# Kernel tuning notes

Measured on AMD Instinct MI355X. Metric: run time of the kernel, lower is better.

Reference implementation:

```python
import jax, jax.numpy as jnp
import numpy as np
from jax import lax

SCALES = [0.5, 0.25, 0.125, 0.0625]
D_MODEL = 256
IN_CH = 1


def setup_inputs() -> dict:
    key = jax.random.key(0)
    ks = jax.random.split(key, 16)
    x = jax.random.normal(ks[0], (2, D_MODEL, 256, 256), dtype=jnp.float32)
    m = jax.random.uniform(ks[1], (2, IN_CH, 256, 256), dtype=jnp.float32)
    s = 0.05
    Wq = jax.random.normal(ks[2], (D_MODEL, D_MODEL, 1, 1), jnp.float32) * s
    bq = jax.random.normal(ks[3], (D_MODEL,), jnp.float32) * s
    Wk = jax.random.normal(ks[4], (D_MODEL, D_MODEL, 1, 1), jnp.float32) * s
    bk = jax.random.normal(ks[5], (D_MODEL,), jnp.float32) * s
    Wv = jax.random.normal(ks[6], (D_MODEL, D_MODEL, 1, 1), jnp.float32) * s
    bv = jax.random.normal(ks[7], (D_MODEL,), jnp.float32) * s
    Wmq = jax.random.normal(ks[8], (D_MODEL, IN_CH, 1, 1), jnp.float32) * s
    bmq = jax.random.normal(ks[9], (D_MODEL,), jnp.float32) * s
    Wmk = jax.random.normal(ks[10], (D_MODEL, IN_CH, 1, 1), jnp.float32) * s
    bmk = jax.random.normal(ks[11], (D_MODEL,), jnp.float32) * s
    Wo = jax.random.normal(ks[12], (D_MODEL, D_MODEL, 3, 3), jnp.float32) * s
    bo = jax.random.normal(ks[13], (D_MODEL,), jnp.float32) * s
    return {"x": x, "m": m, "Wq": Wq, "bq": bq, "Wk": Wk, "bk": bk,
            "Wv": Wv, "bv": bv, "Wmq": Wmq, "bmq": bmq, "Wmk": Wmk, "bmk": bmk,
            "Wo": Wo, "bo": bo, "b": 1, "c": 256}


def _conv1x1(z, W, bias):
    # W: (O, I, 1, 1)
    return jnp.einsum('bihw,oi->bohw', z, W[:, :, 0, 0]) + bias[None, :, None, None]


def _forward(x, m, Wq, bq, Wk, bk, Wv, bv, Wmq, bmq, Wmk, bmk, Wo, bo, b, c):
    bt, _, h, w = x.shape  # h, w are multiples of 64 -> pad is zero
    t = bt // b
    n_scales = len(SCALES)
    d_k = c // n_scales

    q = _conv1x1(x, Wq, bq)
    k = _conv1x1(x, Wk, bk)
    v = _conv1x1(x, Wv, bv)
    mq = _conv1x1(m, Wmq, bmq)
    mk = _conv1x1(m, Wmk, bmk)

    outs = []
    for i, scale in enumerate(SCALES):
        height, width = int(h * scale), int(w * scale)
        out_h, out_w = h // height, w // width
        sl = slice(i * d_k, (i + 1) * d_k)

        def patch(z):
            # (b, t, d_k, out_h, height, out_w, width) -> (b, t*out_h*out_w, d_k*height*width)
            z = z[:, sl].reshape(b, t, d_k, out_h, height, out_w, width)
            z = z.transpose(0, 1, 3, 5, 2, 4, 6)
            return z.reshape(b, t * out_h * out_w, d_k * height * width)

        Q, K, V = patch(q), patch(k), patch(v)
        MQ, MK = patch(mq), patch(mk)
        inv_sqrt_d = 1.0 / jnp.sqrt(jnp.asarray(Q.shape[-1], jnp.float32))
        scores = jnp.einsum('bnd,bmd->bnm', Q, K) * inv_sqrt_d
        mask_scores = jnp.einsum('bnd,bmd->bnm', MQ, MK) * inv_sqrt_d
        p_attn = jax.nn.softmax(scores * mask_scores, axis=-1)
        y = jnp.einsum('bnm,bmd->bnd', p_attn, V)
        # back to (bt, d_k, h, w)
        y = y.reshape(b, t, out_h, out_w, d_k, height, width)
        y = y.transpose(0, 1, 4, 2, 5, 3, 6).reshape(bt, d_k, h, w)
        outs.append(y)

    out = jnp.concatenate(outs, axis=1)
    z = lax.conv_general_dilated(out, Wo, window_strides=(1, 1),
                                 padding=((1, 1), (1, 1)),
                                 dimension_numbers=('NCHW', 'OIHW', 'NCHW'))
    z = z + bo[None, :, None, None]
    return jnp.where(z > 0, z, 0.2 * z)  # LeakyReLU(0.2)


def reference(x, m, Wq, bq, Wk, bk, Wv, bv, Wmq, bmq, Wmk, bmk, Wo, bo, b, c):
    return _forward(x, m, Wq, bq, Wk, bk, Wv, bv, Wmq, bmq, Wmk, bmk, Wo, bo, b, c)
```

## Files before the change

### kernel.cpp

```cpp
#include <hip/hip_runtime.h>
#include <stdint.h>


typedef __attribute__((ext_vector_type(8))) short short8;
typedef __attribute__((ext_vector_type(4))) float floatx4;
typedef __attribute__((ext_vector_type(4))) unsigned int uintx4;

#define DEV static __device__ __forceinline__

DEV unsigned short f2bf(float f) {
  unsigned u = __builtin_bit_cast(unsigned, f);
  unsigned r = u + 0x7FFFu + ((u >> 16) & 1u);
  return (unsigned short)(r >> 16);
}

DEV void patch_row(int n, int sc, int lw, int& pt, int& sp0) {
  pt = n >> (2 + 2 * sc);
  int rem = n & ((4 << (2 * sc)) - 1);
  int oh = rem >> (1 + sc), ow = rem & ((2 << sc) - 1);
  sp0 = (oh << (lw + 8)) + (ow << lw);
}

__global__ void k_prep_w(const float* __restrict__ Wq, const float* __restrict__ Wk,
                         const float* __restrict__ Wv, const float* __restrict__ bq,
                         const float* __restrict__ bk, const float* __restrict__ bv,
                         const float* __restrict__ Wmq, const float* __restrict__ bmq,
                         const float* __restrict__ Wmk, const float* __restrict__ bmk,
                         unsigned short* __restrict__ wqkv, float* __restrict__ bias,
                         float* __restrict__ msc) {
  int b = blockIdx.x;
  int t = threadIdx.x;
  if (b < 768) {
    const float* src = b < 256 ? (Wq + b * 256) : (b < 512 ? (Wk + (b - 256) * 256)
                                                           : (Wv + (b - 512) * 256));
    wqkv[b * 256 + t] = f2bf(src[t]);
    if (t == 0) bias[b] = b < 256 ? bq[b] : (b < 512 ? bk[b - 256] : bv[b - 512]);
  } else {
    int sc = t >> 6, lane = t & 63;
    int ch = sc * 64 + lane;
    float a0 = Wmq[ch] * Wmk[ch];
    float a1 = Wmq[ch] * bmk[ch];
    float a2 = bmq[ch] * Wmk[ch];
    float a3 = bmq[ch] * bmk[ch];
    for (int off = 32; off; off >>= 1) {
      a0 += __shfl_xor(a0, off); a1 += __shfl_xor(a1, off);
      a2 += __shfl_xor(a2, off); a3 += __shfl_xor(a3, off);
    }
    if (lane == 0) {
      msc[sc * 4 + 0] = a0; msc[sc * 4 + 1] = a1;
      msc[sc * 4 + 2] = a2; msc[sc * 4 + 3] = a3;
    }
  }
}

__global__ void k_prep_wo(const float* __restrict__ Wo, unsigned short* __restrict__ wobf,
                          float* __restrict__ scoresG, unsigned int* __restrict__ pbuf) {
  int blk = blockIdx.x;
  if (blk < 2304) {
    int didx = blk >> 8, o = blk & 255, c = threadIdx.x;
    wobf[didx * 65536 + o * 256 + c] = f2bf(Wo[o * 2304 + c * 9 + didx]);
  } else {
    int i = (blk - 2304) * 256 + threadIdx.x;
    if (i < 559232) scoresG[i] = 0.f;
    if (i < 140032) pbuf[i] = 0u;
  }
}

__global__ __launch_bounds__(256) void k_xt(const float* __restrict__ x,
                                            unsigned short* __restrict__ xt) {
  __shared__ __align__(16) unsigned short tile[64][72];
  int p0 = blockIdx.x * 64, c0 = blockIdx.y * 64, t = blockIdx.z;
  int tid = threadIdx.x;
  {
    int cc = tid >> 2, pq = (tid & 3) * 16;
    const float* src = x + ((t * 256 + c0 + cc) * 65536 + p0 + pq);
    __align__(16) unsigned short tmp[16];
#pragma unroll
    for (int e = 0; e < 16; e += 4) {
      floatx4 v = *(const floatx4*)(src + e);
      tmp[e + 0] = f2bf(v[0]); tmp[e + 1] = f2bf(v[1]);
      tmp[e + 2] = f2bf(v[2]); tmp[e + 3] = f2bf(v[3]);
    }
    *(uintx4*)&tile[cc][pq] = *(const uintx4*)&tmp[0];
    *(uintx4*)&tile[cc][pq + 8] = *(const uintx4*)&tmp[8];
  }
  __syncthreads();
  {
    int pp = tid >> 2, cg = (tid & 3) * 16;
    __align__(16) unsigned short outv[16];
#pragma unroll
    for (int e = 0; e < 16; ++e) outv[e] = tile[cg + e][pp];
    unsigned short* dst = xt + ((t * 65536 + p0 + pp) * 256 + c0 + cg);
    *(uintx4*)dst = *(const uintx4*)&outv[0];
    *(uintx4*)(dst + 8) = *(const uintx4*)&outv[8];
  }
}

__global__ __launch_bounds__(256) void k_yt(const unsigned short* __restrict__ ynat,
                                            unsigned short* __restrict__ yt) {
  __shared__ __align__(16) unsigned short tile[64][72];
  int p0 = blockIdx.x * 64, c0 = blockIdx.y * 64, t = blockIdx.z;
  int tid = threadIdx.x;
  {
    int cc = tid >> 2, pq = (tid & 3) * 16;
    const unsigned short* src = ynat + ((t * 256 + c0 + cc) * 65536 + p0 + pq);
    *(uintx4*)&tile[cc][pq] = *(const uintx4*)src;
    *(uintx4*)&tile[cc][pq + 8] = *(const uintx4*)(src + 8);
  }
  __syncthreads();
  {
    int pp = tid >> 2, cg = (tid & 3) * 16;
    __align__(16) unsigned short outv[16];
#pragma unroll
    for (int e = 0; e < 16; ++e) outv[e] = tile[cg + e][pp];
    unsigned short* dst = yt + ((t * 65536 + p0 + pp) * 256 + c0 + cg);
    *(uintx4*)dst = *(const uintx4*)&outv[0];
    *(uintx4*)(dst + 8) = *(const uintx4*)&outv[8];
  }
}

__global__ __launch_bounds__(256) void k_qkv(const unsigned short* __restrict__ xt,
                                             const unsigned short* __restrict__ wqkv,
                                             const float* __restrict__ bias,
                                             unsigned short* __restrict__ qkv) {
  __shared__ __align__(16) unsigned short As[128][64];
  __shared__ __align__(16) unsigned short Bs[128][64];
  int flat = blockIdx.x + (blockIdx.y << 10);
  int lg = ((flat & 7) * 768) + (flat >> 3);
  int n_t = lg / 6, m_t = lg - n_t * 6;
  int n0 = n_t << 7, m0 = m_t << 7;
  int tid = threadIdx.x;
  int w = tid >> 6, l = tid & 63;
  int wr = w >> 1, wc = w & 1;
  int l15 = l & 15, lhi = l >> 4;
  int sr = tid >> 1, sbase = (tid & 1) * 4, r7 = sr & 7;
  const unsigned short* gA = wqkv + (m0 + sr) * 256 + sbase * 8;
  const unsigned short* gB = xt + (n0 + sr) * 256 + sbase * 8;
  floatx4 zf = {0.f, 0.f, 0.f, 0.f};
  floatx4 acc[4][4];
#pragma unroll
  for (int i = 0; i < 4; ++i)
#pragma unroll
    for (int j = 0; j < 4; ++j) acc[i][j] = zf;
  uintx4 ra[4], rb[4];
#define QLOAD(K0) { const uintx4* pa = (const uintx4*)(gA + (K0)); \
                    const uintx4* pb = (const uintx4*)(gB + (K0)); \
                    ra[0] = pa[0]; ra[1] = pa[1]; ra[2] = pa[2]; ra[3] = pa[3]; \
                    rb[0] = pb[0]; rb[1] = pb[1]; rb[2] = pb[2]; rb[3] = pb[3]; }
  QLOAD(0);
#pragma unroll
  for (int ch = 0; ch < 4; ++ch) {
    __syncthreads();
#pragma unroll
    for (int j = 0; j < 4; ++j) {
      *(uintx4*)&As[sr][((sbase + j) ^ r7) * 8] = ra[j];
      *(uintx4*)&Bs[sr][((sbase + j) ^ r7) * 8] = rb[j];
    }
    __syncthreads();
    if (ch < 3) QLOAD((ch + 1) * 64);
#pragma unroll
    for (int kk = 0; kk < 2; ++kk) {
      short8 af[4], bfr[4];
#pragma unroll
      for (int f = 0; f < 4; ++f) {
        int arow = wr * 64 + f * 16 + l15;
        af[f] = *(const short8*)&As[arow][(((kk << 2) + lhi) ^ (arow & 7)) * 8];
        int brow = wc * 64 + f * 16 + l15;
        bfr[f] = *(const short8*)&Bs[brow][(((kk << 2) + lhi) ^ (brow & 7)) * 8];
      }
#pragma unroll
      for (int fm = 0; fm < 4; ++fm)
#pragma unroll
        for (int fn = 0; fn < 4; ++fn)
          acc[fm][fn] = __builtin_amdgcn_mfma_f32_16x16x32_bf16(af[fm], bfr[fn], acc[fm][fn], 0, 0, 0);
    }
  }
#undef QLOAD
#pragma unroll
  for (int fm = 0; fm < 4; ++fm) {
    int crow = m0 + wr * 64 + fm * 16 + lhi * 4;
#pragma unroll
    for (int rr = 0; rr < 4; ++rr) {
      float bv = bias[crow + rr];
#pragma unroll
      for (int fn = 0; fn < 4; ++fn) {
        int pcol = n0 + wc * 64 + fn * 16 + l15;
        int t = pcol >> 16, p = pcol & 65535;
        qkv[(t * 768 + crow + rr) * 65536 + p] = f2bf(acc[fm][fn][rr] + bv);
      }
    }
  }
}

__global__ __launch_bounds__(256) void k_gram2(const float* __restrict__ m,
                                               float* __restrict__ G) {
  __shared__ __align__(16) float Ns[32][68];
  __shared__ __align__(16) float Ms[32][68];
  int bid = blockIdx.x;
  int sc, tn, tm, z, nchunks, soff;
  if (bid < 32)      { sc = 0; tn = 0; tm = 0; z = bid;      nchunks = 8; soff = 0; }
  else if (bid < 40) { sc = 1; tn = 0; tm = 0; z = bid - 32; nchunks = 8; soff = 64; }
  else if (bid < 72) { int r = bid - 40; int tl = r >> 1; sc = 2; tn = tl >> 2; tm = tl & 3; z = r & 1; nchunks = 8; soff = 1088; }
  else               { int tl = bid - 72; sc = 3; tn = tl >> 4; tm = tl & 15; z = 0; nchunks = 4; soff = 17472; }
  int lw = 7 - sc, W = 1 << lw, N = 8 << (2 * sc);
  int kbase = z * nchunks * 64;
  int n0 = tn * 32, m0 = tm * 32;
  int tid = threadIdx.x;
  bool isA = tid < 128;
  int u = tid & 127;
  int srow = u >> 2, sslot0 = (u & 3) * 4;
  int grow = (isA ? n0 : m0) + srow;
  bool valid = grow < N;
  int pt = 0, sp0 = 0;
  if (valid) patch_row(grow, sc, lw, pt, sp0);
  int gbase = pt * 65536 + sp0;
  int trc = tid >> 4, tcc = tid & 15;
  float a00 = 0.f, a01 = 0.f, a10 = 0.f, a11 = 0.f;
  floatx4 zf = {0.f, 0.f, 0.f, 0.f};
  for (int c = 0; c < nchunks; ++c) {
    int k0 = kbase + c * 64;
    floatx4 v[4];
#pragma unroll
    for (int j = 0; j < 4; ++j) {
      v[j] = zf;
      if (valid) {
        int s = k0 + (sslot0 + j) * 4;
        int hh = s >> lw, ww = s & (W - 1);
        v[j] = *(const floatx4*)(m + gbase + (hh << 8) + ww);
      }
    }
    __syncthreads();
    float* dstrow = isA ? &Ns[srow][0] : &Ms[srow][0];
#pragma unroll
    for (int j = 0; j < 4; ++j) *(floatx4*)&dstrow[(sslot0 + j) * 4] = v[j];
    __syncthreads();
#pragma unroll 4
    for (int k = 0; k < 64; k += 4) {
      floatx4 na = *(const floatx4*)&Ns[2 * trc][k];
      floatx4 nb = *(const floatx4*)&Ns[2 * trc + 1][k];
      floatx4 ma = *(const floatx4*)&Ms[2 * tcc][k];
      floatx4 mb = *(const floatx4*)&Ms[2 * tcc + 1][k];
#pragma unroll
      for (int e = 0; e < 4; ++e) {
        a00 += na[e] * ma[e]; a01 += na[e] * mb[e];
        a10 += nb[e] * ma[e]; a11 += nb[e] * mb[e];
      }
    }
  }
  int rn = n0 + 2 * trc, rm = m0 + 2 * tcc;
  float res[2][2] = {{a00, a01}, {a10, a11}};
#pragma unroll
  for (int i = 0; i < 2; ++i)
#pragma unroll
    for (int j = 0; j < 2; ++j) {
      if (rn + i < N && rm + j < N) {
        float* dst = &G[soff + (rn + i) * N + rm + j];
        if (sc < 3) atomicAdd(dst, res[i][j]); else *dst = res[i][j];
      }
    }
}

__global__ void k_rsum(const float* __restrict__ m, float* __restrict__ rbuf) {
  int row = blockIdx.x, lane = threadIdx.x;
  int sc, n;
  if (row < 8)        { sc = 0; n = row; }
  else if (row < 40)  { sc = 1; n = row - 8; }
  else if (row < 168) { sc = 2; n = row - 40; }
  else                { sc = 3; n = row - 168; }
  int lw = 7 - sc, W = 1 << lw;
  int pt, sp0;
  patch_row(n, sc, lw, pt, sp0);
  int base = pt * 65536 + sp0;
  int S = 1 << (14 - 2 * sc);
  float acc = 0.f;
  for (int s = lane; s < S; s += 64) {
    int hh = s >> lw, ww = s & (W - 1);
    acc += m[base + (hh << 8) + ww];
  }
  for (int off = 32; off; off >>= 1) acc += __shfl_xor(acc, off);
  if (lane == 0) rbuf[row] = acc;
}

__global__ __launch_bounds__(256) void k_scores2(const unsigned short* __restrict__ qkv,
                                                 float* __restrict__ scores) {
  __shared__ __align__(16) unsigned short As[32][136];
  __shared__ __align__(16) unsigned short Bs[32][136];
  int bid = blockIdx.x;
  int sc, tn, tm, z, soff;
  if (bid < 256)      { sc = 0; tn = 0; tm = 0; z = bid;       soff = 0; }
  else if (bid < 320) { sc = 1; tn = 0; tm = 0; z = bid - 256; soff = 64; }
  else if (bid < 576) { int r = bid - 320; int tl = r >> 4; sc = 2; tn = tl >> 2; tm = tl & 3; z = r & 15; soff = 1088; }
  else                { int r = bid - 576; int tl = r >> 2; sc = 3; tn = tl >> 4; tm = tl & 15; z = r & 3; soff = 17472; }
  int lw = 7 - sc, W = 1 << lw, lS = 14 - 2 * sc, N = 8 << (2 * sc);
  int n0 = tn * 32, m0 = tm * 32;
  int kbase = z * 4096;
  int tid = threadIdx.x, w = tid >> 6, l = tid & 63;
  int wr = w >> 1, wc = w & 1, l15 = l & 15, lhi = l >> 4;
  floatx4 acc = {0.f, 0.f, 0.f, 0.f};
  bool isA = tid < 128;
  int u = tid & 127;
  int srow = u >> 2, sslot0 = (u & 3) * 4;
  int grow = (isA ? n0 : m0) + srow;
  int cb = (isA ? 0 : 256) + sc * 64;
  int pt = 0, sp0 = 0;
  bool valid = grow < N;
  if (valid) patch_row(grow, sc, lw, pt, sp0);
  int rowbase = (pt * 768 + cb) * 65536 + sp0;
  uintx4 zu = {0u, 0u, 0u, 0u};
  uintx4 r[4];
#define SLOAD(KS) { int kb2 = kbase + (KS) * 128; \
  _Pragma("unroll") for (int j = 0; j < 4; ++j) { \
    uintx4 v = zu; \
    if (valid) { int k = kb2 + (sslot0 + j) * 8; \
      int cl = k >> lS; int s = k & ((1 << lS) - 1); \
      int hh = s >> lw, ww = s & (W - 1); \
      v = *(const uintx4*)(qkv + rowbase + cl * 65536 + (hh << 8) + ww); } \
    r[j] = v; } }
  SLOAD(0);
  for (int ks = 0; ks < 32; ++ks) {
    __syncthreads();
    {
      unsigned short* dstrow = isA ? &As[srow][0] : &Bs[srow][0];
#pragma unroll
      for (int j = 0; j < 4; ++j) *(uintx4*)&dstrow[(sslot0 + j) * 8] = r[j];
    }
    __syncthreads();
    if (ks < 31) SLOAD(ks + 1);
#pragma unroll
    for (int kk = 0; kk < 4; ++kk) {
      short8 a = *(const short8*)&As[wr * 16 + l15][(kk * 4 + lhi) * 8];
      short8 b = *(const short8*)&Bs[wc * 16 + l15][(kk * 4 + lhi) * 8];
      acc = __builtin_amdgcn_mfma_f32_16x16x32_bf16(a, b, acc, 0, 0, 0);
    }
  }
#undef SLOAD
  int rrow = n0 + wr * 16 + lhi * 4;
  int ccol = m0 + wc * 16 + l15;
  if (ccol < N) {
#pragma unroll
    for (int rr = 0; rr < 4; ++rr)
      if (rrow + rr < N) atomicAdd(&scores[soff + (rrow + rr) * N + ccol], acc[rr]);
  }
}

__global__ void k_softmax(const float* __restrict__ scores, const float* __restrict__ G,
                          const float* __restrict__ rbuf, const float* __restrict__ msc,
                          unsigned short* __restrict__ pbuf) {
  int row = blockIdx.x, lane = threadIdx.x;
  int sc, n, roff, soff, poff;
  if (row < 8)        { sc = 0; n = row;       roff = 0;   soff = 0;     poff = 0; }
  else if (row < 40)  { sc = 1; n = row - 8;   roff = 8;   soff = 64;    poff = 512; }
  else if (row < 168) { sc = 2; n = row - 40;  roff = 40;  soff = 1088;  poff = 1536; }
  else                { sc = 3; n = row - 168; roff = 168; soff = 17472; poff = 17920; }
  int N = 8 << (2 * sc);
  int Kpad = (sc < 2) ? 32 : N;
  float Sf = (float)(1 << (14 - 2 * sc));
  float invD = 1.0f / (float)(1 << (20 - 2 * sc));
  float alpha = msc[sc * 4 + 0], beta = msc[sc * 4 + 1];
  float gamma = msc[sc * 4 + 2], delta = msc[sc * 4 + 3];
  float rn = rbuf[roff + n];
  float vals[8];
  float mx = -1e30f;
#pragma unroll
  for (int j = 0; j < 8; ++j) {
    float v = -1e30f;
    int mcol = lane + j * 64;
    if (j * 64 < N && mcol < N) {
      float sq = scores[soff + n * N + mcol];
      float g = G[soff + n * N + mcol];
      float rm = rbuf[roff + mcol];
      v = sq * (alpha * g + beta * rn + gamma * rm + delta * Sf) * invD;
    }
    vals[j] = v;
    mx = fmaxf(mx, v);
  }
  for (int off = 32; off; off >>= 1) mx = fmaxf(mx, __shfl_xor(mx, off));
  float sum = 0.f;
#pragma unroll
  for (int j = 0; j < 8; ++j) {
    int mcol = lane + j * 64;
    float e = 0.f;
    if (j * 64 < N && mcol < N) e = __expf(vals[j] - mx);
    vals[j] = e;
    sum += e;
  }
  for (int off = 32; off; off >>= 1) sum += __shfl_xor(sum, off);
  float inv = 1.f / sum;
#pragma unroll
  for (int j = 0; j < 8; ++j) {
    int mcol = lane + j * 64;
    if (j * 64 < N && mcol < N) pbuf[poff + n * Kpad + mcol] = f2bf(vals[j] * inv);
  }
}

__global__ __launch_bounds__(256) void k_pv(const unsigned short* __restrict__ qkv,
                                            const unsigned short* __restrict__ pbuf,
                                            unsigned short* __restrict__ ynat) {
  int bid = blockIdx.x;
  int sc, bx, by;
  if (bid < 4096)      { sc = 0; bx = bid; by = 0; }
  else if (bid < 6144) { sc = 1; bx = bid - 4096; by = 0; }
  else if (bid < 8192) { int r = bid - 6144; sc = 2; bx = r >> 1; by = r & 1; }
  else                 { int r = bid - 8192; sc = 3; bx = r >> 3; by = r & 7; }
  int WR    = (sc == 0) ? 1 : (sc == 1) ? 2 : 4;
  int logWC = (sc == 0) ? 2 : (sc == 1) ? 1 : 0;
  int poff  = (sc == 0) ? 0 : (sc == 1) ? 512 : (sc == 2) ? 1536 : 17920;
  int lw = 7 - sc, W = 1 << lw;
  int lS = 14 - 2 * sc;
  int N = 8 << (2 * sc);
  int Kpad = (sc < 2) ? 32 : N;
  int WC = 1 << logWC;
  int d0 = bx * (WC * 64);
  int nb = by * (WR * 16);
  __shared__ __align__(16) unsigned short As[64][40];
  __shared__ __align__(16) unsigned short Bt[256][32];
  int tid = threadIdx.x;
  int w = tid >> 6, l = tid & 63;
  int wr = w >> logWC, wc = w & (WC - 1);
  int l15 = l & 15, lhi = l >> 4;
  floatx4 zf = {0.f, 0.f, 0.f, 0.f};
  floatx4 acc[4];
#pragma unroll
  for (int i = 0; i < 4; ++i) acc[i] = zf;
  int bmp = tid & 15;
  int dg = tid >> 4;
  bool act0 = (WC > 1) || (dg < 8);
  bool has1 = (WC == 4);
  bool doA = tid < WR * 64;
  int arow = tid >> 2, akg = (tid & 3) * 8;
  int ksteps = Kpad >> 5;
  uintx4 zu = {0u, 0u, 0u, 0u};
  int vcb = (512 + sc * 64) * 65536;

  for (int ks = 0; ks < ksteps; ++ks) {
    int k0 = ks * 32;
    uintx4 av = zu;
    if (doA) av = *(const uintx4*)(pbuf + poff + (nb + arow) * Kpad + k0 + akg);
    int gm0 = k0 + 2 * bmp, gm1 = gm0 + 1;
    bool mv0 = gm0 < N, mv1 = gm1 < N;
    int pt0 = 0, sp00 = 0, pt1 = 0, sp01 = 0;
    if (mv0) patch_row(gm0, sc, lw, pt0, sp00);
    if (mv1) patch_row(gm1, sc, lw, pt1, sp01);
    uintx4 lo0 = zu, hi0 = zu, lo1 = zu, hi1 = zu;
    {
      int d = d0 + dg * 8;
      int cl = d >> lS;
      int s = d & ((1 << lS) - 1);
      int hh = s >> lw, ww = s & (W - 1);
      int sp = (hh << 8) + ww;
      if (act0 && mv0) lo0 = *(const uintx4*)(qkv + pt0 * 768 * 65536 + vcb + cl * 65536 + sp00 + sp);
      if (act0 && mv1) hi0 = *(const uintx4*)(qkv + pt1 * 768 * 65536 + vcb + cl * 65536 + sp01 + sp);
    }
    if (has1) {
      int d = d0 + (dg + 16) * 8;
      int cl = d >> lS;
      int s = d & ((1 << lS) - 1);
      int hh = s >> lw, ww = s & (W - 1);
      int sp = (hh << 8) + ww;
      if (mv0) lo1 = *(const uintx4*)(qkv + pt0 * 768 * 65536 + vcb + cl * 65536 + sp00 + sp);
      if (mv1) hi1 = *(const uintx4*)(qkv + pt1 * 768 * 65536 + vcb + cl * 65536 + sp01 + sp);
    }
    __syncthreads();
    if (doA) *(uintx4*)&As[arow][akg] = av;
    if (act0) {
      int du = dg * 8;
#pragma unroll
      for (int j = 0; j < 8; ++j) {
        int d = du + j;
        unsigned losh = (lo0[j >> 1] >> ((j & 1) * 16)) & 0xFFFFu;
        unsigned hish = (hi0[j >> 1] >> ((j & 1) * 16)) & 0xFFFFu;
        unsigned wv = losh | (hish << 16);
        int slot = (bmp >> 2) ^ ((d >> 1) & 3) ^ ((d >> 3) & 3);
        ((unsigned int*)&Bt[d][0])[slot * 4 + (bmp & 3)] = wv;
      }
    }
    if (has1) {
      int du = (dg + 16) * 8;
#pragma unroll
      for (int j = 0; j < 8; ++j) {
        int d = du + j;
        unsigned losh = (lo1[j >> 1] >> ((j & 1) * 16)) & 0xFFFFu;
        unsigned hish = (hi1[j >> 1] >> ((j & 1) * 16)) & 0xFFFFu;
        unsigned wv = losh | (hish << 16);
        int slot = (bmp >> 2) ^ ((d >> 1) & 3) ^ ((d >> 3) & 3);
        ((unsigned int*)&Bt[d][0])[slot * 4 + (bmp & 3)] = wv;
      }
    }
    __syncthreads();
    short8 a = *(const short8*)&As[wr * 16 + l15][lhi * 8];
#pragma unroll
    for (int fn = 0; fn < 4; ++fn) {
      int row = wc * 64 + fn * 16 + l15;
      int slot = lhi ^ ((row >> 1) & 3) ^ ((row >> 3) & 3);
      short8 b = *(const short8*)&Bt[row][slot * 8];
      acc[fn] = __builtin_amdgcn_mfma_f32_16x16x32_bf16(a, b, acc[fn], 0, 0, 0);
    }
    __syncthreads();
  }
  int nrow = nb + wr * 16 + lhi * 4;
#pragma unroll
  for (int rr = 0; rr < 4; ++rr) {
    int n = nrow + rr;
    if (n < N) {
      int pt, sp0;
      patch_row(n, sc, lw, pt, sp0);
#pragma unroll
      for (int fn = 0; fn < 4; ++fn) {
        int d = d0 + wc * 64 + fn * 16 + l15;
        int cl = d >> lS;
        int s = d & ((1 << lS) - 1);
        int hh = s >> lw, ww = s & (W - 1);
        int c = sc * 64 + cl;
        ynat[(pt * 256 + c) * 65536 + sp0 + (hh << 8) + ww] = f2bf(acc[fn][rr]);
      }
    }
  }
}

__global__ __launch_bounds__(256, 2) void k_conv(const unsigned short* __restrict__ yt,
                                                 const unsigned short* __restrict__ wo,
                                                 const float* __restrict__ bo,
                                                 float* __restrict__ out) {
  __shared__ __align__(16) unsigned short As[128][128];
  __shared__ __align__(16) unsigned short Bs[130][64];
  int flat = blockIdx.x;
  int lg = ((flat & 7) << 7) + (flat >> 3);
  int n_t = lg >> 1, m_t = lg & 1;
  int n0 = n_t << 8, m0 = m_t << 7;
  int tt = n0 >> 16, yy = (n0 >> 8) & 255;
  int tid = threadIdx.x;
  int w = tid >> 6, l = tid & 63;
  int wr = w >> 1, wc = w & 1;
  int l15 = l & 15, lhi = l >> 4;
  int a_d0 = tid >> 7, a_o0 = tid & 127;
  bool doA1 = tid < 128;
  bool doBh = tid >= 254;
  floatx4 zf = {0.f, 0.f, 0.f, 0.f};
  floatx4 acc[4][8];
#pragma unroll
  for (int i = 0; i < 4; ++i)
#pragma unroll
    for (int j = 0; j < 8; ++j) acc[i][j] = zf;
  uintx4 zu = {0u, 0u, 0u, 0u};
  uintx4 rb[4], ra0[4], ra1[4];
  const unsigned short* ybase = yt + (tt << 24);
#define CLOAD(ST) { \
    int dy = (ST) >> 3, cc = ((ST) & 7) << 5; \
    int yq = yy + dy - 1; \
    bool yv = (unsigned)yq < 256u; \
    { int xq = tid - 1; \
      if (yv && (unsigned)xq < 256u) { \
        const uintx4* p = (const uintx4*)(ybase + ((yq << 8) + xq) * 256 + cc); \
        rb[0] = p[0]; rb[1] = p[1]; rb[2] = p[2]; rb[3] = p[3]; \
      } else { rb[0] = zu; rb[1] = zu; rb[2] = zu; rb[3] = zu; } } \
    { const uintx4* p = (const uintx4*)(wo + (dy * 3 + a_d0) * 65536 + (m0 + a_o0) * 256 + cc); \
      ra0[0] = p[0]; ra0[1] = p[1]; ra0[2] = p[2]; ra0[3] = p[3]; } \
    if (doA1) { \
      const uintx4* p = (const uintx4*)(wo + (dy * 3 + 2) * 65536 + (m0 + tid) * 256 + cc); \
      ra1[0] = p[0]; ra1[1] = p[1]; ra1[2] = p[2]; ra1[3] = p[3]; \
    } else if (doBh) { \
      int xq = tid + 1;   \
      if (yv && xq < 256) { \
        const uintx4* p = (const uintx4*)(ybase + ((yq << 8) + xq) * 256 + cc); \
        ra1[0] = p[0]; ra1[1] = p[1]; ra1[2] = p[2]; ra1[3] = p[3]; \
      } else { ra1[0] = zu; ra1[1] = zu; ra1[2] = zu; ra1[3] = zu; } } }
  CLOAD(0);
  for (int st = 0; st < 24; ++st) {
    __syncthreads();
    {
      int brow = tid >> 1, bhf = (tid & 1) * 4, br7 = brow & 7;
#pragma unroll
      for (int j = 0; j < 4; ++j)
        *(uintx4*)&Bs[brow][((bhf + j) ^ br7) * 8] = rb[j];
      int ao7 = a_o0 & 7;
#pragma unroll
      for (int j = 0; j < 4; ++j)
        *(uintx4*)&As[a_o0][((a_d0 * 4 + j) ^ ao7) * 8] = ra0[j];
      if (doA1) {
        int o7 = tid & 7;
#pragma unroll
        for (int j = 0; j < 4; ++j)
          *(uintx4*)&As[tid][((8 + j) ^ o7) * 8] = ra1[j];
      } else if (doBh) {
        int xh = tid + 2;
        int brow2 = xh >> 1, bhf2 = (xh & 1) * 4, br72 = brow2 & 7;
#pragma unroll
        for (int j = 0; j < 4; ++j)
          *(uintx4*)&Bs[brow2][((bhf2 + j) ^ br72) * 8] = ra1[j];
      }
    }
    __syncthreads();
    if (st < 23) CLOAD(st + 1);
#pragma unroll
    for (int dx = 0; dx < 3; ++dx) {
      short8 af[4];
#pragma unroll
      for (int f = 0; f < 4; ++f) {
        int ol = wr * 64 + f * 16 + l15;
        af[f] = *(const short8*)&As[ol][((dx * 4 + lhi) ^ (ol & 7)) * 8];
      }
#pragma unroll
      for (int fn = 0; fn < 8; ++fn) {
        int xh = wc * 128 + fn * 16 + l15 + dx;
        short8 b = *(const short8*)&Bs[xh >> 1][((((xh & 1) * 4 + lhi)) ^ ((xh >> 1) & 7)) * 8];
#pragma unroll
        for (int fm = 0; fm < 4; ++fm)
          acc[fm][fn] = __builtin_amdgcn_mfma_f32_16x16x32_bf16(af[fm], b, acc[fm][fn], 0, 0, 0);
      }
    }
  }
#undef CLOAD
#pragma unroll
  for (int fm = 0; fm < 4; ++fm) {
    int o = m0 + wr * 64 + fm * 16 + lhi * 4;
#pragma unroll
    for (int rr = 0; rr < 4; ++rr) {
      float bias = bo[o + rr];
#pragma unroll
      for (int fn = 0; fn < 8; ++fn) {
        int xcol = wc * 128 + fn * 16 + l15;
        float z = acc[fm][fn][rr] + bias;
        out[((tt * 256 + o + rr) << 16) + (yy << 8) + xcol] = z > 0.f ? z : 0.2f * z;
      }
    }
  }
}

extern "C" void kernel_launch(void* const* d_in, const int* in_sizes, int n_in,
                              void* d_out, int out_size, void* d_ws, size_t ws_size,
                              hipStream_t stream) {
  const float* x   = (const float*)d_in[0];
  const float* m   = (const float*)d_in[1];
  const float* Wq  = (const float*)d_in[2];
  const float* bq  = (const float*)d_in[3];
  const float* Wk  = (const float*)d_in[4];
  const float* bk  = (const float*)d_in[5];
  const float* Wv  = (const float*)d_in[6];
  const float* bv  = (const float*)d_in[7];
  const float* Wmq = (const float*)d_in[8];
  const float* bmq = (const float*)d_in[9];
  const float* Wmk = (const float*)d_in[10];
  const float* bmk = (const float*)d_in[11];
  const float* Wo  = (const float*)d_in[12];
  const float* bo  = (const float*)d_in[13];

  char* ws = (char*)d_ws;
  unsigned short* qkv   = (unsigned short*)(ws);
  unsigned short* xt    = (unsigned short*)(ws + 201326592);
  unsigned short* wqkv  = (unsigned short*)(ws + 268435456);
  unsigned short* wobf  = (unsigned short*)(ws + 268828672);
  float* bias           = (float*)(ws + 270008320);
  float* msc            = (float*)(ws + 270011392);
  float* scores         = (float*)(ws + 270011456);
  float* G              = (float*)(ws + 271129920);
  float* rbuf           = (float*)(ws + 272248384);
  unsigned short* pbuf  = (unsigned short*)(ws + 272251104);
  float* out            = (float*)d_out;
  unsigned short* ynat  = (unsigned short*)d_out;
  unsigned short* yt    = xt;

  k_prep_w<<<dim3(769), dim3(256), 0, stream>>>(Wq, Wk, Wv, bq, bk, bv, Wmq, bmq, Wmk, bmk,
                                                wqkv, bias, msc);
  k_prep_wo<<<dim3(4489), dim3(256), 0, stream>>>(Wo, wobf, scores, (unsigned int*)pbuf);
  k_xt<<<dim3(1024, 4, 2), dim3(256), 0, stream>>>(x, xt);
  k_qkv<<<dim3(1024, 6), dim3(256), 0, stream>>>(xt, wqkv, bias, qkv);
  k_gram2<<<dim3(328), dim3(256), 0, stream>>>(m, G);
  k_rsum<<<dim3(680), dim3(64), 0, stream>>>(m, rbuf);
  k_scores2<<<dim3(1600), dim3(256), 0, stream>>>(qkv, scores);
  k_softmax<<<dim3(680), dim3(64), 0, stream>>>(scores, G, rbuf, msc, pbuf);
  k_pv<<<dim3(10240), dim3(256), 0, stream>>>(qkv, pbuf, ynat);
  k_yt<<<dim3(1024, 4, 2), dim3(256), 0, stream>>>(ynat, yt);
  k_conv<<<dim3(1024), dim3(256), 0, stream>>>(yt, wobf, bo, out);
}
```

Measured before the change: 568.4 us.

## Fuse x transpose into QKV GEMM, add big-tile scores kernel, double-buffer PV

Removes the separate x transpose/convert kernel: the QKV GEMM now reads fp32 x directly, converts it to bf16 in registers and scatters it into swizzled shared memory. Scales 2 and 3 of the score computation move to a new 128x128-tile MFMA kernel with split-K atomics, replacing the small 32x32 tiles. The PV kernel gains double-buffered shared memory with prefetch of the next K step, which drops a barrier per iteration. In exchange, the fused load does many scalar LDS stores, and the new score tiling uses fewer, larger blocks with more atomics per block.

Result: slower. 627.2 us (+10.3%).

```diff
diff --git a/kernel.cpp b/kernel.cpp
--- a/kernel.cpp
+++ b/kernel.cpp
@@ -66,36 +66,6 @@
   }
 }
 
-__global__ __launch_bounds__(256) void k_xt(const float* __restrict__ x,
-                                            unsigned short* __restrict__ xt) {
-  __shared__ __align__(16) unsigned short tile[64][72];
-  int p0 = blockIdx.x * 64, c0 = blockIdx.y * 64, t = blockIdx.z;
-  int tid = threadIdx.x;
-  {
-    int cc = tid >> 2, pq = (tid & 3) * 16;
-    const float* src = x + ((t * 256 + c0 + cc) * 65536 + p0 + pq);
-    __align__(16) unsigned short tmp[16];
-#pragma unroll
-    for (int e = 0; e < 16; e += 4) {
-      floatx4 v = *(const floatx4*)(src + e);
-      tmp[e + 0] = f2bf(v[0]); tmp[e + 1] = f2bf(v[1]);
-      tmp[e + 2] = f2bf(v[2]); tmp[e + 3] = f2bf(v[3]);
-    }
-    *(uintx4*)&tile[cc][pq] = *(const uintx4*)&tmp[0];
-    *(uintx4*)&tile[cc][pq + 8] = *(const uintx4*)&tmp[8];
-  }
-  __syncthreads();
-  {
-    int pp = tid >> 2, cg = (tid & 3) * 16;
-    __align__(16) unsigned short outv[16];
-#pragma unroll
-    for (int e = 0; e < 16; ++e) outv[e] = tile[cg + e][pp];
-    unsigned short* dst = xt + ((t * 65536 + p0 + pp) * 256 + c0 + cg);
-    *(uintx4*)dst = *(const uintx4*)&outv[0];
-    *(uintx4*)(dst + 8) = *(const uintx4*)&outv[8];
-  }
-}
-
 __global__ __launch_bounds__(256) void k_yt(const unsigned short* __restrict__ ynat,
                                             unsigned short* __restrict__ yt) {
   __shared__ __align__(16) unsigned short tile[64][72];
@@ -119,7 +89,7 @@
   }
 }
 
-__global__ __launch_bounds__(256) void k_qkv(const unsigned short* __restrict__ xt,
+__global__ __launch_bounds__(256) void k_qkv(const float* __restrict__ x,
                                              const unsigned short* __restrict__ wqkv,
                                              const float* __restrict__ bias,
                                              unsigned short* __restrict__ qkv) {
@@ -135,26 +105,39 @@
   int l15 = l & 15, lhi = l >> 4;
   int sr = tid >> 1, sbase = (tid & 1) * 4, r7 = sr & 7;
   const unsigned short* gA = wqkv + (m0 + sr) * 256 + sbase * 8;
-  const unsigned short* gB = xt + (n0 + sr) * 256 + sbase * 8;
+  int chl = tid & 63, pseg = tid >> 6;
+  int tt = n0 >> 16, pp0 = (n0 & 65535) + pseg * 32;
+  const float* gB = x + ((tt * 256 + chl) * 65536 + pp0);
   floatx4 zf = {0.f, 0.f, 0.f, 0.f};
   floatx4 acc[4][4];
 #pragma unroll
   for (int i = 0; i < 4; ++i)
 #pragma unroll
     for (int j = 0; j < 4; ++j) acc[i][j] = zf;
-  uintx4 ra[4], rb[4];
+  uintx4 ra[4];
+  floatx4 rxb[8];
 #define QLOAD(K0) { const uintx4* pa = (const uintx4*)(gA + (K0)); \
-                    const uintx4* pb = (const uintx4*)(gB + (K0)); \
                     ra[0] = pa[0]; ra[1] = pa[1]; ra[2] = pa[2]; ra[3] = pa[3]; \
-                    rb[0] = pb[0]; rb[1] = pb[1]; rb[2] = pb[2]; rb[3] = pb[3]; }
+                    const float* pb = gB + (K0) * 65536; \
+                    _Pragma("unroll") for (int q = 0; q < 8; ++q) \
+                      rxb[q] = *(const floatx4*)(pb + q * 4); }
   QLOAD(0);
 #pragma unroll
   for (int ch = 0; ch < 4; ++ch) {
-    __syncthreads();
-#pragma unroll
-    for (int j = 0; j < 4; ++j) {
+    __align__(16) unsigned short tmps[32];
+#pragma unroll
+    for (int e = 0; e < 32; ++e) tmps[e] = f2bf(rxb[e >> 2][e & 3]);
+    __syncthreads();
+#pragma unroll
+    for (int j = 0; j < 4; ++j)
       *(uintx4*)&As[sr][((sbase + j) ^ r7) * 8] = ra[j];
-      *(uintx4*)&Bs[sr][((sbase + j) ^ r7) * 8] = rb[j];
+    {
+      int ck = chl >> 3, cw = chl & 7;
+#pragma unroll
+      for (int e = 0; e < 32; ++e) {
+        int p = pseg * 32 + e;
+        Bs[p][((ck ^ (e & 7)) << 3) + cw] = tmps[e];
+      }
     }
     __syncthreads();
     if (ch < 3) QLOAD((ch + 1) * 64);
@@ -288,9 +271,7 @@
   int bid = blockIdx.x;
   int sc, tn, tm, z, soff;
   if (bid < 256)      { sc = 0; tn = 0; tm = 0; z = bid;       soff = 0; }
-  else if (bid < 320) { sc = 1; tn = 0; tm = 0; z = bid - 256; soff = 64; }
-  else if (bid < 576) { int r = bid - 320; int tl = r >> 4; sc = 2; tn = tl >> 2; tm = tl & 3; z = r & 15; soff = 1088; }
-  else                { int r = bid - 576; int tl = r >> 2; sc = 3; tn = tl >> 4; tm = tl & 15; z = r & 3; soff = 17472; }
+  else                { sc = 1; tn = 0; tm = 0; z = bid - 256; soff = 64; }
   int lw = 7 - sc, W = 1 << lw, lS = 14 - 2 * sc, N = 8 << (2 * sc);
   int n0 = tn * 32, m0 = tm * 32;
   int kbase = z * 4096;
@@ -343,6 +324,86 @@
   }
 }
 
+__global__ __launch_bounds__(256) void k_scores_big(const unsigned short* __restrict__ qkv,
+                                                    float* __restrict__ scores) {
+  __shared__ __align__(16) unsigned short As[128][64];
+  __shared__ __align__(16) unsigned short Bs[128][64];
+  int flat = blockIdx.x;
+  int lg = (flat & 7) * 20 + (flat >> 3);
+  int sc, tn, tm, z, soff;
+  if (lg < 32) { sc = 2; tn = 0; tm = 0; z = lg; soff = 1088; }
+  else { int r = lg - 32; int tl = r >> 3; sc = 3; tn = tl >> 2; tm = tl & 3; z = r & 7; soff = 17472; }
+  int N = 8 << (2 * sc);
+  int lw = 7 - sc, W = 1 << lw, lS = 14 - 2 * sc;
+  int n0 = tn * 128, m0 = tm * 128;
+  int kbase = z * 2048;
+  int tid = threadIdx.x;
+  int w = tid >> 6, l = tid & 63;
+  int wr = w >> 1, wc = w & 1;
+  int l15 = l & 15, lhi = l >> 4;
+  int sr = tid >> 1, sbase = (tid & 1) * 4, r7 = sr & 7;
+  int ptA, spA, ptB, spB;
+  patch_row(n0 + sr, sc, lw, ptA, spA);
+  patch_row(m0 + sr, sc, lw, ptB, spB);
+  int baseA = (ptA * 768 + sc * 64) * 65536 + spA;
+  int baseB = (ptB * 768 + 256 + sc * 64) * 65536 + spB;
+  floatx4 zf = {0.f, 0.f, 0.f, 0.f};
+  floatx4 acc[4][4];
+#pragma unroll
+  for (int i = 0; i < 4; ++i)
+#pragma unroll
+    for (int j = 0; j < 4; ++j) acc[i][j] = zf;
+  uintx4 ra[4], rb[4];
+#define GLOAD(K0) { \
+  _Pragma("unroll") for (int j = 0; j < 4; ++j) { \
+    int k = kbase + (K0) + (sbase + j) * 8; \
+    int cl = k >> lS; int s = k & ((1 << lS) - 1); \
+    int hh = s >> lw, ww = s & (W - 1); \
+    int off = cl * 65536 + (hh << 8) + ww; \
+    ra[j] = *(const uintx4*)(qkv + baseA + off); \
+    rb[j] = *(const uintx4*)(qkv + baseB + off); } }
+  GLOAD(0);
+  for (int st = 0; st < 32; ++st) {
+    __syncthreads();
+#pragma unroll
+    for (int j = 0; j < 4; ++j) {
+      *(uintx4*)&As[sr][((sbase + j) ^ r7) * 8] = ra[j];
+      *(uintx4*)&Bs[sr][((sbase + j) ^ r7) * 8] = rb[j];
+    }
+    __syncthreads();
+    if (st < 31) GLOAD((st + 1) * 64);
+#pragma unroll
+    for (int kk = 0; kk < 2; ++kk) {
+      short8 af[4], bfr[4];
+#pragma unroll
+      for (int f = 0; f < 4; ++f) {
+        int arow = wr * 64 + f * 16 + l15;
+        af[f] = *(const short8*)&As[arow][(((kk << 2) + lhi) ^ (arow & 7)) * 8];
+        int brow = wc * 64 + f * 16 + l15;
+        bfr[f] = *(const short8*)&Bs[brow][(((kk << 2) + lhi) ^ (brow & 7)) * 8];
+      }
+#pragma unroll
+      for (int fm = 0; fm < 4; ++fm)
+#pragma unroll
+        for (int fn = 0; fn < 4; ++fn)
+          acc[fm][fn] = __builtin_amdgcn_mfma_f32_16x16x32_bf16(af[fm], bfr[fn], acc[fm][fn], 0, 0, 0);
+    }
+  }
+#undef GLOAD
+#pragma unroll
+  for (int fm = 0; fm < 4; ++fm) {
+    int nrow = n0 + wr * 64 + fm * 16 + lhi * 4;
+#pragma unroll
+    for (int rr = 0; rr < 4; ++rr) {
+#pragma unroll
+      for (int fn = 0; fn < 4; ++fn) {
+        int mcol = m0 + wc * 64 + fn * 16 + l15;
+        atomicAdd(&scores[soff + (nrow + rr) * N + mcol], acc[fm][fn][rr]);
+      }
+    }
+  }
+}
+
 __global__ void k_softmax(const float* __restrict__ scores, const float* __restrict__ G,
                           const float* __restrict__ rbuf, const float* __restrict__ msc,
                           unsigned short* __restrict__ pbuf) {
@@ -412,8 +473,8 @@
   int WC = 1 << logWC;
   int d0 = bx * (WC * 64);
   int nb = by * (WR * 16);
-  __shared__ __align__(16) unsigned short As[64][40];
-  __shared__ __align__(16) unsigned short Bt[256][32];
+  __shared__ __align__(16) unsigned short As[2][64][40];
+  __shared__ __align__(16) unsigned short Bt[2][256][32];
   int tid = threadIdx.x;
   int w = tid >> 6, l = tid & 63;
   int wr = w >> logWC, wc = w & (WC - 1);
@@ -431,37 +492,27 @@
   int ksteps = Kpad >> 5;
   uintx4 zu = {0u, 0u, 0u, 0u};
   int vcb = (512 + sc * 64) * 65536;
-
+  uintx4 av = zu, lo0 = zu, hi0 = zu, lo1 = zu, hi1 = zu;
+#define PLOADS(KS) { int k0 = (KS) * 32; \
+    av = zu; lo0 = zu; hi0 = zu; lo1 = zu; hi1 = zu; \
+    if (doA) av = *(const uintx4*)(pbuf + poff + (nb + arow) * Kpad + k0 + akg); \
+    int gm0 = k0 + 2 * bmp, gm1 = gm0 + 1; \
+    bool mv0 = gm0 < N, mv1 = gm1 < N; \
+    int pt0 = 0, sp00 = 0, pt1 = 0, sp01 = 0; \
+    if (mv0) patch_row(gm0, sc, lw, pt0, sp00); \
+    if (mv1) patch_row(gm1, sc, lw, pt1, sp01); \
+    { int d = d0 + dg * 8; int cl = d >> lS; int s = d & ((1 << lS) - 1); \
+      int hh = s >> lw, ww = s & (W - 1); int sp = (hh << 8) + ww; \
+      if (act0 && mv0) lo0 = *(const uintx4*)(qkv + pt0 * 768 * 65536 + vcb + cl * 65536 + sp00 + sp); \
+      if (act0 && mv1) hi0 = *(const uintx4*)(qkv + pt1 * 768 * 65536 + vcb + cl * 65536 + sp01 + sp); } \
+    if (has1) { int d = d0 + (dg + 16) * 8; int cl = d >> lS; int s = d & ((1 << lS) - 1); \
+      int hh = s >> lw, ww = s & (W - 1); int sp = (hh << 8) + ww; \
+      if (mv0) lo1 = *(const uintx4*)(qkv + pt0 * 768 * 65536 + vcb + cl * 65536 + sp00 + sp); \
+      if (mv1) hi1 = *(const uintx4*)(qkv + pt1 * 768 * 65536 + vcb + cl * 65536 + sp01 + sp); } }
+  PLOADS(0);
   for (int ks = 0; ks < ksteps; ++ks) {
-    int k0 = ks * 32;
-    uintx4 av = zu;
-    if (doA) av = *(const uintx4*)(pbuf + poff + (nb + arow) * Kpad + k0 + akg);
-    int gm0 = k0 + 2 * bmp, gm1 = gm0 + 1;
-    bool mv0 = gm0 < N, mv1 = gm1 < N;
-    int pt0 = 0, sp00 = 0, pt1 = 0, sp01 = 0;
-    if (mv0) patch_row(gm0, sc, lw, pt0, sp00);
-    if (mv1) patch_row(gm1, sc, lw, pt1, sp01);
-    uintx4 lo0 = zu, hi0 = zu, lo1 = zu, hi1 = zu;
-    {
-      int d = d0 + dg * 8;
-      int cl = d >> lS;
-      int s = d & ((1 << lS) - 1);
-      int hh = s >> lw, ww = s & (W - 1);
-      int sp = (hh << 8) + ww;
-      if (act0 && mv0) lo0 = *(const uintx4*)(qkv + pt0 * 768 * 65536 + vcb + cl * 65536 + sp00 + sp);
-      if (act0 && mv1) hi0 = *(const uintx4*)(qkv + pt1 * 768 * 65536 + vcb + cl * 65536 + sp01 + sp);
-    }
-    if (has1) {
-      int d = d0 + (dg + 16) * 8;
-      int cl = d >> lS;
-      int s = d & ((1 << lS) - 1);
-      int hh = s >> lw, ww = s & (W - 1);
-      int sp = (hh << 8) + ww;
-      if (mv0) lo1 = *(const uintx4*)(qkv + pt0 * 768 * 65536 + vcb + cl * 65536 + sp00 + sp);
-      if (mv1) hi1 = *(const uintx4*)(qkv + pt1 * 768 * 65536 + vcb + cl * 65536 + sp01 + sp);
-    }
-    __syncthreads();
-    if (doA) *(uintx4*)&As[arow][akg] = av;
+    int b = ks & 1;
+    if (doA) *(uintx4*)&As[b][arow][akg] = av;
     if (act0) {
       int du = dg * 8;
 #pragma unroll
@@ -471,7 +522,7 @@
         unsigned hish = (hi0[j >> 1] >> ((j & 1) * 16)) & 0xFFFFu;
         unsigned wv = losh | (hish << 16);
         int slot = (bmp >> 2) ^ ((d >> 1) & 3) ^ ((d >> 3) & 3);
-        ((unsigned int*)&Bt[d][0])[slot * 4 + (bmp & 3)] = wv;
+        ((unsigned int*)&Bt[b][d][0])[slot * 4 + (bmp & 3)] = wv;
       }
     }
     if (has1) {
@@ -483,20 +534,21 @@
         unsigned hish = (hi1[j >> 1] >> ((j & 1) * 16)) & 0xFFFFu;
         unsigned wv = losh | (hish << 16);
         int slot = (bmp >> 2) ^ ((d >> 1) & 3) ^ ((d >> 3) & 3);
-        ((unsigned int*)&Bt[d][0])[slot * 4 + (bmp & 3)] = wv;
-      }
-    }
-    __syncthreads();
-    short8 a = *(const short8*)&As[wr * 16 + l15][lhi * 8];
+        ((unsigned int*)&Bt[b][d][0])[slot * 4 + (bmp & 3)] = wv;
+      }
+    }
+    __syncthreads();
+    if (ks + 1 < ksteps) PLOADS(ks + 1);
+    short8 a = *(const short8*)&As[b][wr * 16 + l15][lhi * 8];
 #pragma unroll
     for (int fn = 0; fn < 4; ++fn) {
       int row = wc * 64 + fn * 16 + l15;
       int slot = lhi ^ ((row >> 1) & 3) ^ ((row >> 3) & 3);
-      short8 b = *(const short8*)&Bt[row][slot * 8];
-      acc[fn] = __builtin_amdgcn_mfma_f32_16x16x32_bf16(a, b, acc[fn], 0, 0, 0);
-    }
-    __syncthreads();
-  }
+      short8 bb = *(const short8*)&Bt[b][row][slot * 8];
+      acc[fn] = __builtin_amdgcn_mfma_f32_16x16x32_bf16(a, bb, acc[fn], 0, 0, 0);
+    }
+  }
+#undef PLOADS
   int nrow = nb + wr * 16 + lhi * 4;
 #pragma unroll
   for (int rr = 0; rr < 4; ++rr) {
@@ -559,7 +611,7 @@
       const uintx4* p = (const uintx4*)(wo + (dy * 3 + 2) * 65536 + (m0 + tid) * 256 + cc); \
       ra1[0] = p[0]; ra1[1] = p[1]; ra1[2] = p[2]; ra1[3] = p[3]; \
     } else if (doBh) { \
-      int xq = tid + 1;   \
+      int xq = tid + 1; \
       if (yv && xq < 256) { \
         const uintx4* p = (const uintx4*)(ybase + ((yq << 8) + xq) * 256 + cc); \
         ra1[0] = p[0]; ra1[1] = p[1]; ra1[2] = p[2]; ra1[3] = p[3]; \
@@ -646,7 +698,7 @@
 
   char* ws = (char*)d_ws;
   unsigned short* qkv   = (unsigned short*)(ws);
-  unsigned short* xt    = (unsigned short*)(ws + 201326592);
+  unsigned short* ytb   = (unsigned short*)(ws + 201326592);
   unsigned short* wqkv  = (unsigned short*)(ws + 268435456);
   unsigned short* wobf  = (unsigned short*)(ws + 268828672);
   float* bias           = (float*)(ws + 270008320);
@@ -657,18 +709,17 @@
   unsigned short* pbuf  = (unsigned short*)(ws + 272251104);
   float* out            = (float*)d_out;
   unsigned short* ynat  = (unsigned short*)d_out;
-  unsigned short* yt    = xt;
 
   k_prep_w<<<dim3(769), dim3(256), 0, stream>>>(Wq, Wk, Wv, bq, bk, bv, Wmq, bmq, Wmk, bmk,
                                                 wqkv, bias, msc);
   k_prep_wo<<<dim3(4489), dim3(256), 0, stream>>>(Wo, wobf, scores, (unsigned int*)pbuf);
-  k_xt<<<dim3(1024, 4, 2), dim3(256), 0, stream>>>(x, xt);
-  k_qkv<<<dim3(1024, 6), dim3(256), 0, stream>>>(xt, wqkv, bias, qkv);
+  k_qkv<<<dim3(1024, 6), dim3(256), 0, stream>>>(x, wqkv, bias, qkv);
   k_gram2<<<dim3(328), dim3(256), 0, stream>>>(m, G);
   k_rsum<<<dim3(680), dim3(64), 0, stream>>>(m, rbuf);
-  k_scores2<<<dim3(1600), dim3(256), 0, stream>>>(qkv, scores);
+  k_scores2<<<dim3(320), dim3(256), 0, stream>>>(qkv, scores);
+  k_scores_big<<<dim3(160), dim3(256), 0, stream>>>(qkv, scores);
   k_softmax<<<dim3(680), dim3(64), 0, stream>>>(scores, G, rbuf, msc, pbuf);
   k_pv<<<dim3(10240), dim3(256), 0, stream>>>(qkv, pbuf, ynat);
-  k_yt<<<dim3(1024, 4, 2), dim3(256), 0, stream>>>(ynat, yt);
-  k_conv<<<dim3(1024), dim3(256), 0, stream>>>(yt, wobf, bo, out);
-}
+  k_yt<<<dim3(1024, 4, 2), dim3(256), 0, stream>>>(ynat, ytb);
+  k_conv<<<dim3(1024), dim3(256), 0, stream>>>(ytb, wobf, bo, out);
+}
```
